# Performance work log

Measured on AMD Instinct MI355X. Metric: run time of the kernel, lower is better.

## Reference

```python
import jax, jax.numpy as jnp
import numpy as np

N_HEAD = 16
MAX_SEQ_LEN = 2048
RATIO = 1
NEG_INF = -jnp.inf


def make_alibi_bias(n_head: int, max_seq_len: int, ratio: int) -> jnp.ndarray:
    # bias[t, s] = s*ratio - t, masked to -inf where > 0 (future positions)
    s = jnp.arange(max_seq_len)[None, :] * ratio            # [1, S]
    t = jnp.arange(max_seq_len * ratio)[:, None]            # [T, 1]
    bias = (s - t).astype(jnp.float32)                      # [T, S]
    bias = jnp.where(bias > 0, NEG_INF, bias)
    # per-head slopes: cumprod of 2^(-8/n_head) -> m_i = 2^(-8*(i+1)/n_head)
    m = jnp.cumprod(jnp.full((n_head,), 2.0 ** (-8.0 / n_head), dtype=jnp.float32))
    return bias[None, :, :] * m[:, None, None]              # [H, T, S]


def setup_inputs() -> dict:
    key = jax.random.key(0)
    kq, kk, kv = jax.random.split(key, 3)
    B, T, D = 2, 2048, 1024
    return {
        "q": jax.random.normal(kq, (B, T, D), dtype=jnp.float32),
        "k": jax.random.normal(kk, (B, T, D), dtype=jnp.float32),
        "v": jax.random.normal(kv, (B, T, D), dtype=jnp.float32),
    }


def reference(q, k, v):
    B, T, D = q.shape
    S = k.shape[1]
    H = N_HEAD
    dh = D // H
    # split heads: [B, T, D] -> [B, H, T, dh]
    qh = q.reshape(B, T, H, dh).transpose(0, 2, 1, 3)
    kh = k.reshape(B, S, H, dh).transpose(0, 2, 1, 3)
    vh = v.reshape(B, S, H, dh).transpose(0, 2, 1, 3)

    scores = jnp.einsum("bhtd,bhsd->bhts", qh, kh) / jnp.sqrt(jnp.float32(dh))
    bias = make_alibi_bias(H, MAX_SEQ_LEN, RATIO)[:, -T:, -S:]  # [H, T, S]
    attn = jax.nn.softmax(scores + bias[None], axis=-1)
    out = jnp.einsum("bhts,bhsd->bhtd", attn, vh)
    # gather heads: [B, H, T, dh] -> [B, T, D]
    return out.transpose(0, 2, 1, 3).reshape(B, T, D)
```

## Files before the change

kernel.cpp:

```cpp
#include <hip/hip_runtime.h>

#define N_HEAD 16
#define DHEAD 64
#define TSEQ 2048
#define DMODEL 1024
#define BATCH 2

typedef _Float16 f16x8 __attribute__((ext_vector_type(8)));
typedef _Float16 f16x4 __attribute__((ext_vector_type(4)));
typedef _Float16 f16x2 __attribute__((ext_vector_type(2)));
typedef __fp16 fp16x2 __attribute__((ext_vector_type(2)));
typedef float f32x4 __attribute__((ext_vector_type(4)));

union F8 { f16x8 v; uint4 u; f16x2 h[4]; };
union F4 { f16x4 v; uint2 u; f16x2 h[2]; };

#if __has_builtin(__builtin_amdgcn_exp2f)
#define EXP2F(x) __builtin_amdgcn_exp2f(x)
#else
#define EXP2F(x) exp2f(x)
#endif

__device__ __forceinline__ void gload_lds16(const void* g, void* l) {
    __builtin_amdgcn_global_load_lds(
        (const __attribute__((address_space(1))) void*)g,
        (__attribute__((address_space(3))) void*)l, 16, 0, 0);
}

__device__ __forceinline__ f16x2 pk(float a, float b) {
    union { fp16x2 i; f16x2 o; } c;
    c.i = __builtin_amdgcn_cvt_pkrtz(a, b);
    return c.o;
}

__device__ __forceinline__ F8 pack8_f32(const float* p) {
    const float4 a = *(const float4*)p;
    const float4 b = *(const float4*)(p + 4);
    F8 r;
    r.h[0] = pk(a.x, a.y); r.h[1] = pk(a.z, a.w);
    r.h[2] = pk(b.x, b.y); r.h[3] = pk(b.z, b.w);
    return r;
}

__global__ __launch_bounds__(256) void prep(const float* __restrict__ K,
                                            const float* __restrict__ V,
                                            _Float16* __restrict__ Kh,
                                            _Float16* __restrict__ Vh)
{
    __shared__ float tl[64][67];
    const int bh = blockIdx.y, b = bh >> 4, h = bh & 15;
    const int s0 = blockIdx.x * 64;
    const int t = threadIdx.x;
    const int r16 = t >> 4, c4 = (t & 15) * 4;
    #pragma unroll
    for (int pass = 0; pass < 4; ++pass) {
        const int row = pass * 16 + r16;
        const size_t goff = ((size_t)(b * TSEQ + s0 + row)) * DMODEL + h * DHEAD + c4;
        const float4 fk = *(const float4*)(K + goff);
        F4 ok;
        ok.h[0] = pk(fk.x, fk.y);
        ok.h[1] = pk(fk.z, fk.w);
        *(uint2*)(Kh + (((size_t)bh * TSEQ + s0 + row) << 6) + c4) = ok.u;
        const float4 fv = *(const float4*)(V + goff);
        tl[row][c4 + 0] = fv.x; tl[row][c4 + 1] = fv.y;
        tl[row][c4 + 2] = fv.z; tl[row][c4 + 3] = fv.w;
    }
    __syncthreads();
    const int d = t >> 2, sc = (t & 3) * 16;
    F8 p0, p1;
    #pragma unroll
    for (int j = 0; j < 4; ++j) p0.h[j] = pk(tl[sc + 2 * j][d], tl[sc + 2 * j + 1][d]);
    #pragma unroll
    for (int j = 0; j < 4; ++j) p1.h[j] = pk(tl[sc + 8 + 2 * j][d], tl[sc + 9 + 2 * j][d]);
    _Float16* vo = Vh + ((size_t)bh * DHEAD + d) * TSEQ + s0 + sc;
    *(uint4*)vo = p0.u;
    *(uint4*)(vo + 8) = p1.u;
}

__global__ __launch_bounds__(256, 2) void alibi_attn(
    const float* __restrict__ Q, const _Float16* __restrict__ Kh,
    const _Float16* __restrict__ Vh, float* __restrict__ O)
{
    __shared__ __align__(16) char kbuf[2][8192];
    __shared__ __align__(16) char vbuf[2][8192];

    const int wv   = threadIdx.x >> 6;
    const int lane = threadIdx.x & 63;
    const int quad = lane >> 4;
    const int l16  = lane & 15;

    const int bh = blockIdx.x;
    const int b  = bh >> 4, h = bh & 15;
    const int px = blockIdx.y;

    const float LOG2E   = 1.44269504088896f;
    const float slope   = exp2f(-0.5f * (float)(h + 1));
    const float bslope2 = slope * LOG2E;
    const float sscale2 = 0.125f * LOG2E;
    const float step64  = 64.0f * bslope2;
    const float rb1 = bslope2, rb2 = 2.f * bslope2, rb3 = 3.f * bslope2;

    const float* qp  = Q + (size_t)b * TSEQ * DMODEL + (size_t)h * DHEAD;
    const char*  kpb = (const char*)(Kh + (size_t)bh * TSEQ * DHEAD);
    const char*  vpb = (const char*)(Vh + (size_t)bh * DHEAD * TSEQ);

    const int st_r  = lane >> 3;
    const int k_src = st_r * 128  + (((lane & 7) ^ st_r) * 16);
    const int v_src = st_r * 4096 + (((lane & 7) ^ st_r) * 16);

    const int koff0 = l16 * 128 + ((quad ^ (l16 & 7)) * 16);
    const int koff1 = l16 * 128 + (((quad + 4) ^ (l16 & 7)) * 16);
    const int vbase = l16 * 128 + (quad & 1) * 8;
    int vx[4];
    #pragma unroll
    for (int sj = 0; sj < 4; ++sj)
        vx[sj] = ((sj * 2 + (quad >> 1)) ^ (l16 & 7)) * 16;

    const f32x4 zero4 = {0.f, 0.f, 0.f, 0.f};

    for (int hp = 0; hp < 2; ++hp) {
        const int sx     = hp ? (31 - px) : px;
        const int base_w = sx * 64 + wv * 16;

        auto stage = [&](int t) {
            const char* kg = kpb + (size_t)t * 8192;
            const char* vg = vpb + (size_t)t * 128;
            char* kd = kbuf[t & 1];
            char* vd = vbuf[t & 1];
            #pragma unroll
            for (int c = 0; c < 2; ++c) {
                const int gr = wv * 16 + c * 8;
                gload_lds16(kg + gr * 128 + k_src, kd + gr * 128);
                gload_lds16(vg + gr * 4096 + v_src, vd + gr * 128);
            }
        };

        stage(0);

        const float* qr = qp + (size_t)(base_w + l16) * DMODEL + quad * 8;
        const F8 aq0 = pack8_f32(qr);
        const F8 aq1 = pack8_f32(qr + 32);

        f32x4 o[4];
        float lp = 0.f;
        float dbq[4];
        #pragma unroll
        for (int nt = 0; nt < 4; ++nt) o[nt] = zero4;
        #pragma unroll
        for (int sj = 0; sj < 4; ++sj)
            dbq[sj] = (float)(sj * 16 + quad * 4 - base_w - l16) * bslope2;

        __syncthreads();

        for (int t = 0; t <= sx; ++t) {
            if (t < sx) stage(t + 1);
            const char* kb = kbuf[t & 1];
            const char* vb = vbuf[t & 1];

            F8 kA[4][2];
            #pragma unroll
            for (int sj = 0; sj < 4; ++sj) {
                kA[sj][0].u = *(const uint4*)(kb + sj * 2048 + koff0);
                kA[sj][1].u = *(const uint4*)(kb + sj * 2048 + koff1);
            }

            f32x4 sT[4];
            #pragma unroll
            for (int sj = 0; sj < 4; ++sj) {
                f32x4 acc = zero4;
                acc = __builtin_amdgcn_mfma_f32_16x16x32_f16(kA[sj][0].v, aq0.v, acc, 0, 0, 0);
                acc = __builtin_amdgcn_mfma_f32_16x16x32_f16(kA[sj][1].v, aq1.v, acc, 0, 0, 0);
                sT[sj] = acc;
            }

            F4 vf[4][4];
            #pragma unroll
            for (int nt = 0; nt < 4; ++nt)
                #pragma unroll
                for (int sj = 0; sj < 4; ++sj)
                    vf[nt][sj].u = *(const uint2*)(vb + nt * 2048 + vbase + vx[sj]);

            const bool masked = (t == sx);
            F4 pP[4];
            #pragma unroll
            for (int sj = 0; sj < 4; ++sj) {
                const float db = dbq[sj];
                float p0 = EXP2F(fmaf(sT[sj][0], sscale2, db));
                float p1 = EXP2F(fmaf(sT[sj][1], sscale2, db + rb1));
                float p2 = EXP2F(fmaf(sT[sj][2], sscale2, db + rb2));
                float p3 = EXP2F(fmaf(sT[sj][3], sscale2, db + rb3));
                if (masked) {
                    const int di = t * 64 + sj * 16 + quad * 4 - base_w - l16;
                    if (di + 0 > 0) p0 = 0.f;
                    if (di + 1 > 0) p1 = 0.f;
                    if (di + 2 > 0) p2 = 0.f;
                    if (di + 3 > 0) p3 = 0.f;
                }
                lp += (p0 + p1) + (p2 + p3);
                pP[sj].h[0] = pk(p0, p1);
                pP[sj].h[1] = pk(p2, p3);
                dbq[sj] = db + step64;
            }

            #pragma unroll
            for (int nt = 0; nt < 4; ++nt)
                #pragma unroll
                for (int sj = 0; sj < 4; ++sj)
                    o[nt] = __builtin_amdgcn_mfma_f32_16x16x16f16(
                        pP[sj].v, vf[nt][sj].v, o[nt], 0, 0, 0);

            __syncthreads();
        }

        float ls = lp;
        ls += __shfl_xor(ls, 16);
        ls += __shfl_xor(ls, 32);
        float lr[4];
        #pragma unroll
        for (int r = 0; r < 4; ++r)
            lr[r] = __shfl(ls, quad * 4 + r);
        #pragma unroll
        for (int nt = 0; nt < 4; ++nt)
            #pragma unroll
            for (int r = 0; r < 4; ++r) {
                const int trow = base_w + quad * 4 + r;
                O[((size_t)b * TSEQ + trow) * DMODEL + h * DHEAD + nt * 16 + l16] =
                    o[nt][r] / lr[r];
            }
    }
}

extern "C" void kernel_launch(void* const* d_in, const int* in_sizes, int n_in,
                              void* d_out, int out_size, void* d_ws, size_t ws_size,
                              hipStream_t stream) {
    const float* q = (const float*)d_in[0];
    const float* k = (const float*)d_in[1];
    const float* v = (const float*)d_in[2];
    float* out = (float*)d_out;

    _Float16* Kh = (_Float16*)d_ws;
    _Float16* Vh = Kh + (size_t)BATCH * N_HEAD * TSEQ * DHEAD;

    prep<<<dim3(TSEQ / 64, BATCH * N_HEAD), 256, 0, stream>>>(k, v, Kh, Vh);
    alibi_attn<<<dim3(BATCH * N_HEAD, 16), 256, 0, stream>>>(q, Kh, Vh, out);
}
```

Measured before the change: 129.0 us.

## Process two adjacent query tiles per block sharing K/V tile loads

Each block now handles two consecutive 64-row query tiles (128 rows) and streams K/V tiles once for both, replacing the previous pairing of a short and a long query tile that were processed one after the other. This halves LDS staging and global K/V reads per query row and doubles MFMA work per barrier. Block order is permuted so the heaviest tiles launch first, and s_setprio is raised around the MFMA sections to favour matrix issue. The cost is a larger register footprint (two accumulator sets and two Q fragments), which may limit occupancy at two blocks per CU, plus less even per-block work.

```diff
diff --git a/kernel.cpp b/kernel.cpp
--- a/kernel.cpp
+++ b/kernel.cpp
@@ -91,7 +91,9 @@
 
     const int bh = blockIdx.x;
     const int b  = bh >> 4, h = bh & 15;
-    const int px = blockIdx.y;
+    const int py = blockIdx.y;
+    const int qt = (py < 8) ? (15 - py) : (py - 8);
+    const int sx2 = 2 * qt + 1;
 
     const float LOG2E   = 1.44269504088896f;
     const float slope   = exp2f(-0.5f * (float)(h + 1));
@@ -118,101 +120,158 @@
 
     const f32x4 zero4 = {0.f, 0.f, 0.f, 0.f};
 
-    for (int hp = 0; hp < 2; ++hp) {
-        const int sx     = hp ? (31 - px) : px;
-        const int base_w = sx * 64 + wv * 16;
-
-        auto stage = [&](int t) {
-            const char* kg = kpb + (size_t)t * 8192;
-            const char* vg = vpb + (size_t)t * 128;
-            char* kd = kbuf[t & 1];
-            char* vd = vbuf[t & 1];
-            #pragma unroll
-            for (int c = 0; c < 2; ++c) {
-                const int gr = wv * 16 + c * 8;
-                gload_lds16(kg + gr * 128 + k_src, kd + gr * 128);
-                gload_lds16(vg + gr * 4096 + v_src, vd + gr * 128);
-            }
-        };
-
-        stage(0);
-
-        const float* qr = qp + (size_t)(base_w + l16) * DMODEL + quad * 8;
-        const F8 aq0 = pack8_f32(qr);
-        const F8 aq1 = pack8_f32(qr + 32);
-
-        f32x4 o[4];
-        float lp = 0.f;
-        float dbq[4];
-        #pragma unroll
-        for (int nt = 0; nt < 4; ++nt) o[nt] = zero4;
-        #pragma unroll
-        for (int sj = 0; sj < 4; ++sj)
-            dbq[sj] = (float)(sj * 16 + quad * 4 - base_w - l16) * bslope2;
-
-        __syncthreads();
-
-        for (int t = 0; t <= sx; ++t) {
-            if (t < sx) stage(t + 1);
-            const char* kb = kbuf[t & 1];
-            const char* vb = vbuf[t & 1];
-
-            F8 kA[4][2];
-            #pragma unroll
-            for (int sj = 0; sj < 4; ++sj) {
-                kA[sj][0].u = *(const uint4*)(kb + sj * 2048 + koff0);
-                kA[sj][1].u = *(const uint4*)(kb + sj * 2048 + koff1);
-            }
-
-            f32x4 sT[4];
+    const int base0 = qt * 128 + wv * 16;
+    const int base1 = base0 + 64;
+
+    auto stage = [&](int t) {
+        const char* kg = kpb + (size_t)t * 8192;
+        const char* vg = vpb + (size_t)t * 128;
+        char* kd = kbuf[t & 1];
+        char* vd = vbuf[t & 1];
+        #pragma unroll
+        for (int c = 0; c < 2; ++c) {
+            const int gr = wv * 16 + c * 8;
+            gload_lds16(kg + gr * 128 + k_src, kd + gr * 128);
+            gload_lds16(vg + gr * 4096 + v_src, vd + gr * 128);
+        }
+    };
+
+    stage(0);
+
+    const float* qr0 = qp + (size_t)(base0 + l16) * DMODEL + quad * 8;
+    const float* qr1 = qp + (size_t)(base1 + l16) * DMODEL + quad * 8;
+    const F8 aq00 = pack8_f32(qr0);
+    const F8 aq01 = pack8_f32(qr0 + 32);
+    const F8 aq10 = pack8_f32(qr1);
+    const F8 aq11 = pack8_f32(qr1 + 32);
+
+    f32x4 o0[4], o1[4];
+    float lp0 = 0.f, lp1 = 0.f;
+    float dbq0[4], dbq1[4];
+    #pragma unroll
+    for (int nt = 0; nt < 4; ++nt) { o0[nt] = zero4; o1[nt] = zero4; }
+    #pragma unroll
+    for (int sj = 0; sj < 4; ++sj) {
+        dbq0[sj] = (float)(sj * 16 + quad * 4 - base0 - l16) * bslope2;
+        dbq1[sj] = (float)(sj * 16 + quad * 4 - base1 - l16) * bslope2;
+    }
+
+    __syncthreads();
+
+    for (int t = 0; t <= sx2; ++t) {
+        if (t < sx2) stage(t + 1);
+        const char* kb = kbuf[t & 1];
+        const char* vb = vbuf[t & 1];
+
+        F8 kA[4][2];
+        #pragma unroll
+        for (int sj = 0; sj < 4; ++sj) {
+            kA[sj][0].u = *(const uint4*)(kb + sj * 2048 + koff0);
+            kA[sj][1].u = *(const uint4*)(kb + sj * 2048 + koff1);
+        }
+
+        const bool run0 = (t < sx2);
+
+        f32x4 sT0[4], sT1[4];
+        __builtin_amdgcn_s_setprio(1);
+        if (run0) {
             #pragma unroll
             for (int sj = 0; sj < 4; ++sj) {
                 f32x4 acc = zero4;
-                acc = __builtin_amdgcn_mfma_f32_16x16x32_f16(kA[sj][0].v, aq0.v, acc, 0, 0, 0);
-                acc = __builtin_amdgcn_mfma_f32_16x16x32_f16(kA[sj][1].v, aq1.v, acc, 0, 0, 0);
-                sT[sj] = acc;
+                acc = __builtin_amdgcn_mfma_f32_16x16x32_f16(kA[sj][0].v, aq00.v, acc, 0, 0, 0);
+                acc = __builtin_amdgcn_mfma_f32_16x16x32_f16(kA[sj][1].v, aq01.v, acc, 0, 0, 0);
+                sT0[sj] = acc;
             }
-
-            F4 vf[4][4];
-            #pragma unroll
-            for (int nt = 0; nt < 4; ++nt)
-                #pragma unroll
-                for (int sj = 0; sj < 4; ++sj)
-                    vf[nt][sj].u = *(const uint2*)(vb + nt * 2048 + vbase + vx[sj]);
-
-            const bool masked = (t == sx);
+        }
+        #pragma unroll
+        for (int sj = 0; sj < 4; ++sj) {
+            f32x4 acc = zero4;
+            acc = __builtin_amdgcn_mfma_f32_16x16x32_f16(kA[sj][0].v, aq10.v, acc, 0, 0, 0);
+            acc = __builtin_amdgcn_mfma_f32_16x16x32_f16(kA[sj][1].v, aq11.v, acc, 0, 0, 0);
+            sT1[sj] = acc;
+        }
+        __builtin_amdgcn_s_setprio(0);
+
+        F4 vf[4][4];
+        #pragma unroll
+        for (int nt = 0; nt < 4; ++nt)
+            #pragma unroll
+            for (int sj = 0; sj < 4; ++sj)
+                vf[nt][sj].u = *(const uint2*)(vb + nt * 2048 + vbase + vx[sj]);
+
+        if (run0) {
+            const bool masked = (t == sx2 - 1);
             F4 pP[4];
             #pragma unroll
             for (int sj = 0; sj < 4; ++sj) {
-                const float db = dbq[sj];
-                float p0 = EXP2F(fmaf(sT[sj][0], sscale2, db));
-                float p1 = EXP2F(fmaf(sT[sj][1], sscale2, db + rb1));
-                float p2 = EXP2F(fmaf(sT[sj][2], sscale2, db + rb2));
-                float p3 = EXP2F(fmaf(sT[sj][3], sscale2, db + rb3));
+                const float db = dbq0[sj];
+                float p0 = EXP2F(fmaf(sT0[sj][0], sscale2, db));
+                float p1 = EXP2F(fmaf(sT0[sj][1], sscale2, db + rb1));
+                float p2 = EXP2F(fmaf(sT0[sj][2], sscale2, db + rb2));
+                float p3 = EXP2F(fmaf(sT0[sj][3], sscale2, db + rb3));
                 if (masked) {
-                    const int di = t * 64 + sj * 16 + quad * 4 - base_w - l16;
+                    const int di = t * 64 + sj * 16 + quad * 4 - base0 - l16;
                     if (di + 0 > 0) p0 = 0.f;
                     if (di + 1 > 0) p1 = 0.f;
                     if (di + 2 > 0) p2 = 0.f;
                     if (di + 3 > 0) p3 = 0.f;
                 }
-                lp += (p0 + p1) + (p2 + p3);
+                lp0 += (p0 + p1) + (p2 + p3);
                 pP[sj].h[0] = pk(p0, p1);
                 pP[sj].h[1] = pk(p2, p3);
-                dbq[sj] = db + step64;
+                dbq0[sj] = db + step64;
             }
-
+            __builtin_amdgcn_s_setprio(1);
             #pragma unroll
             for (int nt = 0; nt < 4; ++nt)
                 #pragma unroll
                 for (int sj = 0; sj < 4; ++sj)
-                    o[nt] = __builtin_amdgcn_mfma_f32_16x16x16f16(
-                        pP[sj].v, vf[nt][sj].v, o[nt], 0, 0, 0);
-
-            __syncthreads();
-        }
-
-        float ls = lp;
+                    o0[nt] = __builtin_amdgcn_mfma_f32_16x16x16f16(
+                        pP[sj].v, vf[nt][sj].v, o0[nt], 0, 0, 0);
+            __builtin_amdgcn_s_setprio(0);
+        }
+
+        {
+            const bool masked = (t == sx2);
+            F4 pP[4];
+            #pragma unroll
+            for (int sj = 0; sj < 4; ++sj) {
+                const float db = dbq1[sj];
+                float p0 = EXP2F(fmaf(sT1[sj][0], sscale2, db));
+                float p1 = EXP2F(fmaf(sT1[sj][1], sscale2, db + rb1));
+                float p2 = EXP2F(fmaf(sT1[sj][2], sscale2, db + rb2));
+                float p3 = EXP2F(fmaf(sT1[sj][3], sscale2, db + rb3));
+                if (masked) {
+                    const int di = t * 64 + sj * 16 + quad * 4 - base1 - l16;
+                    if (di + 0 > 0) p0 = 0.f;
+                    if (di + 1 > 0) p1 = 0.f;
+                    if (di + 2 > 0) p2 = 0.f;
+                    if (di + 3 > 0) p3 = 0.f;
+                }
+                lp1 += (p0 + p1) + (p2 + p3);
+                pP[sj].h[0] = pk(p0, p1);
+                pP[sj].h[1] = pk(p2, p3);
+                dbq1[sj] = db + step64;
+            }
+            __builtin_amdgcn_s_setprio(1);
+            #pragma unroll
+            for (int nt = 0; nt < 4; ++nt)
+                #pragma unroll
+                for (int sj = 0; sj < 4; ++sj)
+                    o1[nt] = __builtin_amdgcn_mfma_f32_16x16x16f16(
+                        pP[sj].v, vf[nt][sj].v, o1[nt], 0, 0, 0);
+            __builtin_amdgcn_s_setprio(0);
+        }
+
+        __syncthreads();
+    }
+
+    #pragma unroll
+    for (int m = 0; m < 2; ++m) {
+        const float lpm  = m ? lp1 : lp0;
+        const f32x4* om  = m ? o1 : o0;
+        const int base_m = m ? base1 : base0;
+        float ls = lpm;
         ls += __shfl_xor(ls, 16);
         ls += __shfl_xor(ls, 32);
         float lr[4];
@@ -223,9 +282,9 @@
         for (int nt = 0; nt < 4; ++nt)
             #pragma unroll
             for (int r = 0; r < 4; ++r) {
-                const int trow = base_w + quad * 4 + r;
+                const int trow = base_m + quad * 4 + r;
                 O[((size_t)b * TSEQ + trow) * DMODEL + h * DHEAD + nt * 16 + l16] =
-                    o[nt][r] / lr[r];
+                    om[nt][r] / lr[r];
             }
     }
 }
```

Result: slower. 141.4 us (+9.6%).
